# Kernel optimization log

Hardware: AMD Instinct MI355X
Metric: run time of the kernel (lower is better)

## Reference

```python
import jax, jax.numpy as jnp
import numpy as np

F_DIM = 128; K_RBF = 64; NBLOCKS = 3; NUM_SCC = 1; IBEGIN = 4
N_RES_INT = 2; N_RES_AT = 2; N_RES_OUT = 1
NUM_OUTPUTS = 2001; NOUTS = NUM_OUTPUTS + 4  # +4 charge-equilibration channels when num_scc>0
N_ATOMS = 10000; DEG = 32; N_EDGES = N_ATOMS * DEG; NMOL = 64
CUTOFF = 10.0
LOG2 = 0.6931471805599453


def ssp(x):
    # shifted softplus
    return jax.nn.softplus(x) - LOG2


def _residual(x, W1, b1, W2, b2):
    y = ssp(x) @ W1 + b1
    return x + ssp(y) @ W2 + b2


def _forward(R, M, QaAlpha, QaBeta,
             em_W0, em_b0, em_W1, em_b1, em_W2, em_b2,
             iWrbf, iWi, ibi, iWj, ibj, irW1, irb1, irW2, irb2, iWout, ibout, iu,
             arW1, arb1, arW2, arb2, orW1, orb1, orW2, orb2, oW,
             Z, idx_i, idx_j, mol_idx):
    N = R.shape[0]
    dt = R.dtype
    # --- interatomic distances via neighbor gather ---
    Dvec = R[idx_i] - R[idx_j]                                # [E,3]
    Dij = jnp.sqrt(jax.nn.relu(jnp.sum(Dvec * Dvec, -1)))     # [E]
    # --- PhysNet-style exp-Gaussian RBF expansion with smooth cutoff ---
    mu = jnp.linspace(np.exp(-CUTOFF), 1.0, K_RBF).astype(dt)
    gamma = jnp.asarray((K_RBF / (2.0 * (1.0 - np.exp(-CUTOFF)))) ** 2, dt)
    t = Dij / CUTOFF
    cut = jnp.where(Dij < CUTOFF, 1.0 - 6.0 * t**5 + 15.0 * t**4 - 10.0 * t**3, 0.0)
    rbf = cut[:, None] * jnp.exp(-gamma * (jnp.exp(-Dij)[:, None] - mu) ** 2)  # [E,K]

    seg_mol = lambda v: jax.ops.segment_sum(v, mol_idx, num_segments=NMOL)
    Zf = Z.astype(dt)[:, None]
    QaA, QaB = QaAlpha, QaBeta
    QAlpha_mol = seg_mol(QaA)
    QBeta_mol = seg_mol(QaB)
    outputs = None
    nhloss = jnp.asarray(0.0, dt)
    for j in range(NUM_SCC + 1):
        # elemental-modes embedding: f = [Z, M, QaAlpha, QaBeta] -> F
        f = jnp.concatenate([Zf, M[:, None], QaA[:, None], QaB[:, None]], 1)  # [N,4]
        h = ssp(f @ em_W0 + em_b0)
        h = ssp(h @ em_W1 + em_b1)
        x = h @ em_W2 + em_b2                                 # [N,F]
        outputs = jnp.zeros((N, NOUTS), dt)
        nhloss = jnp.asarray(0.0, dt)
        lastout2 = None
        for i in range(NBLOCKS):
            # --- interaction (message passing: gather -> multiply -> segment_sum) ---
            xa = ssp(x)
            g = rbf @ iWrbf[i]                                # [E,F]
            xi = ssp(xa @ iWi[i] + ibi[i])                    # [N,F]
            xj = ssp(xa @ iWj[i] + ibj[i])                    # [N,F]
            m = xi + jax.ops.segment_sum(g * xj[idx_j], idx_i, num_segments=N)
            for r in range(N_RES_INT):
                m = _residual(m, irW1[i, r], irb1[i, r], irW2[i, r], irb2[i, r])
            m = ssp(m)
            x = iu[i] * x + m @ iWout[i] + ibout[i]           # gated update
            for r in range(N_RES_AT):
                x = _residual(x, arW1[i, r], arb1[i, r], arW2[i, r], arb2[i, r])
            # --- output block ---
            xo = x
            for r in range(N_RES_OUT):
                xo = _residual(xo, orW1[i, r], orb1[i, r], orW2[i, r], orb2[i, r])
            out = ssp(xo) @ oW[i]                             # [N,NOUTS]
            outputs = outputs + out
            if j == NUM_SCC:
                out2 = out[IBEGIN:] ** 2                      # row slice, as in source
                if i > 0:
                    nhloss = nhloss + jnp.mean(out2 / (out2 + lastout2 + 1e-7))
                lastout2 = out2
        # --- NSE charge equilibration (per-molecule segment sums) ---
        QaA_n, faA = outputs[:, 0], outputs[:, 1]
        QaB_n, faB = outputs[:, 2], outputs[:, 3]
        QaA = QaA_n + faA * ((QAlpha_mol - seg_mol(QaA_n)) / seg_mol(faA))[mol_idx]
        QaB = QaB_n + faB * ((QBeta_mol - seg_mol(QaB_n)) / seg_mol(faB))[mol_idx]
    outputs = outputs[:, IBEGIN:]
    outputs = jnp.concatenate([outputs[:, :1], jax.nn.relu(outputs[:, 1:])], 1)
    return outputs, Dij, nhloss


def setup_inputs() -> dict:
    key = jax.random.key(0)
    ks = iter(jax.random.split(key, 64))
    nrm = lambda shp, scale: jax.random.normal(next(ks), shp, jnp.float32) * scale
    F, K, B = F_DIM, K_RBF, NBLOCKS
    s = F ** -0.5
    inp = {}
    inp["R"] = jax.random.uniform(next(ks), (N_ATOMS, 3), jnp.float32, 0.0, 12.0)
    inp["M"] = jax.random.uniform(next(ks), (N_ATOMS,), jnp.float32, 1.0, 32.0)
    inp["QaAlpha"] = nrm((N_ATOMS,), 0.1)
    inp["QaBeta"] = nrm((N_ATOMS,), 0.1)
    # elemental-modes MLP 4 -> F -> F -> F
    inp["em_W0"] = nrm((4, F), 0.5); inp["em_b0"] = nrm((F,), 0.01)
    inp["em_W1"] = nrm((F, F), s);   inp["em_b1"] = nrm((F,), 0.01)
    inp["em_W2"] = nrm((F, F), s);   inp["em_b2"] = nrm((F,), 0.01)
    # interaction blocks (stacked over NBLOCKS)
    inp["iWrbf"] = nrm((B, K, F), K ** -0.5)
    inp["iWi"] = nrm((B, F, F), s); inp["ibi"] = nrm((B, F), 0.01)
    inp["iWj"] = nrm((B, F, F), s); inp["ibj"] = nrm((B, F), 0.01)
    inp["irW1"] = nrm((B, N_RES_INT, F, F), s); inp["irb1"] = nrm((B, N_RES_INT, F), 0.01)
    inp["irW2"] = nrm((B, N_RES_INT, F, F), s); inp["irb2"] = nrm((B, N_RES_INT, F), 0.01)
    inp["iWout"] = nrm((B, F, F), s); inp["ibout"] = nrm((B, F), 0.01)
    inp["iu"] = jnp.ones((B, F), jnp.float32)
    inp["arW1"] = nrm((B, N_RES_AT, F, F), s); inp["arb1"] = nrm((B, N_RES_AT, F), 0.01)
    inp["arW2"] = nrm((B, N_RES_AT, F, F), s); inp["arb2"] = nrm((B, N_RES_AT, F), 0.01)
    inp["orW1"] = nrm((B, N_RES_OUT, F, F), s); inp["orb1"] = nrm((B, N_RES_OUT, F), 0.01)
    inp["orW2"] = nrm((B, N_RES_OUT, F, F), s); inp["orb2"] = nrm((B, N_RES_OUT, F), 0.01)
    inp["oW"] = nrm((B, F, NOUTS), s)
    # integer graph structure
    inp["Z"] = jax.random.randint(next(ks), (N_ATOMS,), 1, 36, jnp.int32)
    idx_i = jnp.repeat(jnp.arange(N_ATOMS, dtype=jnp.int32), DEG)
    rnd = jax.random.randint(next(ks), (N_EDGES,), 1, N_ATOMS, jnp.int32)
    inp["idx_i"] = idx_i
    inp["idx_j"] = (idx_i + rnd) % N_ATOMS  # never self -> Dij > 0
    inp["mol_idx"] = ((jnp.arange(N_ATOMS) * NMOL) // N_ATOMS).astype(jnp.int32)
    return inp


def reference(R, M, QaAlpha, QaBeta,
              em_W0, em_b0, em_W1, em_b1, em_W2, em_b2,
              iWrbf, iWi, ibi, iWj, ibj, irW1, irb1, irW2, irb2, iWout, ibout, iu,
              arW1, arb1, arW2, arb2, orW1, orb1, orW2, orb2, oW,
              Z, idx_i, idx_j, mol_idx):
    return _forward(R, M, QaAlpha, QaBeta,
                    em_W0, em_b0, em_W1, em_b1, em_W2, em_b2,
                    iWrbf, iWi, ibi, iWj, ibj, irW1, irb1, irW2, irb2, iWout, ibout, iu,
                    arW1, arb1, arW2, arb2, orW1, orb1, orW2, orb2, oW,
                    Z, idx_i, idx_j, mol_idx)
```

## Files before the change

### kernel.cpp

```cpp
#include <hip/hip_runtime.h>
#include <math.h>

#define NA 10000
#define FD 128
#define KR 64
#define DEGC 32
#define NE (NA*DEGC)
#define NOUTS_C 2005
#define NOUT_FINAL 2001

typedef __attribute__((ext_vector_type(8))) short bh8;
typedef __attribute__((ext_vector_type(4))) float fx4;

__device__ __forceinline__ float sspf(float x){
    float ex = __expf(-fabsf(x));
    return fmaxf(x, 0.0f) + __logf(1.0f + ex) - 0.6931471805599453f;
}
__device__ __forceinline__ unsigned short f2bf(float x){
    unsigned int u = __float_as_uint(x);
    unsigned int r = (u + 0x7fffu + ((u >> 16) & 1u)) >> 16;
    return (unsigned short)r;
}
__device__ __forceinline__ float bf2f(unsigned short u){
    return __uint_as_float(((unsigned int)u) << 16);
}
__device__ __forceinline__ fx4 mfma16(bh8 a, bh8 b, fx4 c){
    return __builtin_amdgcn_mfma_f32_16x16x32_bf16(a, b, c, 0, 0, 0);
}
__device__ __forceinline__ void gll16(const void* g, void* l){
    __builtin_amdgcn_global_load_lds(
        (const __attribute__((address_space(1))) unsigned int*)g,
        (__attribute__((address_space(3))) unsigned int*)l, 16, 0, 0);
}

__global__ void k_dij(const float* __restrict__ R, const int* __restrict__ idx_i,
                      const int* __restrict__ idx_j, float* __restrict__ dij_out){
    int e = blockIdx.x*256 + threadIdx.x;
    if (e >= NE) return;
    int i = idx_i[e], j = idx_j[e];
    float dx = R[i*3+0] - R[j*3+0];
    float dy = R[i*3+1] - R[j*3+1];
    float dz = R[i*3+2] - R[j*3+2];
    dij_out[e] = sqrtf(fmaxf(dx*dx + dy*dy + dz*dz, 0.0f));
}

__global__ void k_init(const float* __restrict__ QaAin, const float* __restrict__ QaBin,
                       const int* __restrict__ mol, float* __restrict__ QaA,
                       float* __restrict__ QaB, float* __restrict__ QAmol,
                       float* __restrict__ QBmol){
    int a = blockIdx.x*256 + threadIdx.x;
    if (a >= NA) return;
    float qa = QaAin[a], qb = QaBin[a];
    QaA[a] = qa; QaB[a] = qb;
    int m = mol[a];
    atomicAdd(&QAmol[m], qa);
    atomicAdd(&QBmol[m], qb);
}

__global__ void k_cvtW(const float* __restrict__ em_W1, const float* __restrict__ em_W2,
                       const float* __restrict__ iWi, const float* __restrict__ iWj,
                       const float* __restrict__ iWout, const float* __restrict__ irW1,
                       const float* __restrict__ irW2, const float* __restrict__ arW1,
                       const float* __restrict__ arW2, const float* __restrict__ orW1,
                       const float* __restrict__ orW2, short* __restrict__ img){
    int gid = blockIdx.x*256 + threadIdx.x;
    if (gid >= 41*2048) return;
    int m = gid >> 11;
    int f = gid & 2047;
    int l15 = f & 15, t = f >> 4;
    int g = t & 3, u = t >> 2;
    int kk = u & 3, cg = u >> 2;
    const float* src; int mm;
    if      (m < 1){ src = em_W1; mm = m; }
    else if (m < 2){ src = em_W2; mm = m-1; }
    else if (m < 5){ src = iWi;   mm = m-2; }
    else if (m < 8){ src = iWj;   mm = m-5; }
    else if (m < 11){ src = iWout; mm = m-8; }
    else if (m < 17){ src = irW1;  mm = m-11; }
    else if (m < 23){ src = irW2;  mm = m-17; }
    else if (m < 29){ src = arW1;  mm = m-23; }
    else if (m < 35){ src = arW2;  mm = m-29; }
    else if (m < 38){ src = orW1;  mm = m-35; }
    else            { src = orW2;  mm = m-38; }
    src += (size_t)mm * 16384;
    int n = cg*16 + l15;
    int k0 = (kk*4 + g)*8;
    bh8 pk;
    #pragma unroll
    for (int j = 0; j < 8; ++j) pk[j] = (short)f2bf(src[(k0+j)*128 + n]);
    *(bh8*)&img[m*16384 + f*8] = pk;
}

__global__ void k_cvtB(const float* __restrict__ em_b1, const float* __restrict__ em_b2,
                       const float* __restrict__ ibi, const float* __restrict__ ibj,
                       const float* __restrict__ ibout, const float* __restrict__ irb1,
                       const float* __restrict__ irb2, const float* __restrict__ arb1,
                       const float* __restrict__ arb2, const float* __restrict__ orb1,
                       const float* __restrict__ orb2, const float* __restrict__ iu,
                       float* __restrict__ bimg){
    int gid = blockIdx.x*256 + threadIdx.x;
    if (gid >= 44*128) return;
    int m = gid >> 7, c = gid & 127;
    float v;
    if      (m < 1)  v = em_b1[c];
    else if (m < 2)  v = em_b2[c];
    else if (m < 5)  v = ibi[(m-2)*128+c];
    else if (m < 8)  v = ibj[(m-5)*128+c];
    else if (m < 11) v = ibout[(m-8)*128+c];
    else if (m < 17) v = irb1[(m-11)*128+c];
    else if (m < 23) v = irb2[(m-17)*128+c];
    else if (m < 29) v = arb1[(m-23)*128+c];
    else if (m < 35) v = arb2[(m-29)*128+c];
    else if (m < 38) v = orb1[(m-35)*128+c];
    else if (m < 41) v = orb2[(m-38)*128+c];
    else             v = iu[(m-41)*128+c];
    bimg[gid] = v;
}

__global__ void k_cvt_wrbf(const float* __restrict__ iWrbf, short* __restrict__ img){
    int gid = blockIdx.x*256 + threadIdx.x;
    if (gid >= 3*1024) return;
    int i = gid >> 10;
    int loc = gid & 1023;
    int n = loc >> 3, s = loc & 7;
    const float* src = iWrbf + (size_t)i*8192;
    int kbase = (s ^ (n&7)) * 8;
    bh8 pk;
    #pragma unroll
    for (int j = 0; j < 8; ++j) pk[j] = (short)f2bf(src[(kbase+j)*128 + n]);
    *(bh8*)&img[i*8192 + n*64 + s*8] = pk;
}

__global__ void k_cvt_oW(const float* __restrict__ oW, short* __restrict__ img){
    int gid = blockIdx.x*256 + threadIdx.x;
    if (gid >= 98304) return;
    int l15 = gid & 15;
    int g = (gid >> 4) & 3;
    int nt = (gid >> 6) & 7;
    int rest = gid >> 9;
    int kk2 = rest % 12, cg = rest / 12;
    int seg = kk2 >> 2;
    int n = cg*128 + nt*16 + l15;
    int kbase = (kk2 & 3)*32 + g*8;
    bh8 pk;
    #pragma unroll
    for (int j = 0; j < 8; ++j){
        float v = (n < NOUTS_C) ? oW[((size_t)seg*128 + kbase + j)*NOUTS_C + n] : 0.0f;
        pk[j] = (short)f2bf(v);
    }
    *(bh8*)&img[(size_t)gid*8] = pk;
}

__device__ __forceinline__ void loadB8(const short* __restrict__ W, int g, int l15, int wv, bh8 b[8]){
    const bh8* Wf = (const bh8*)W;
    const int cgA = wv*2, cgB = wv*2 + 1;
    #pragma unroll
    for (int kk = 0; kk < 4; ++kk){
        b[kk]   = Wf[((cgA*4+kk)*4+g)*16 + l15];
        b[4+kk] = Wf[((cgB*4+kk)*4+g)*16 + l15];
    }
}
__device__ __forceinline__ void gemmB(const short* As, const bh8 b[8], int g, int l15, fx4 acc[2]){
    #pragma unroll
    for (int kk = 0; kk < 4; ++kk){
        int q = kk*4 + g;
        bh8 a = *(const bh8*)&As[l15*128 + ((q ^ (l15&7))*8)];
        acc[0] = mfma16(a, b[kk],   acc[0]);
        acc[1] = mfma16(a, b[4+kk], acc[1]);
    }
}
#define ZACC2 { acc[0]=(fx4){0,0,0,0}; acc[1]=(fx4){0,0,0,0}; }

__device__ __forceinline__ void epiS_ts(short* dst, fx4 acc[2], const float* b,
                                        int g, int c0, int c1){
    float b0 = b[c0], b1 = b[c1];
    #pragma unroll
    for (int r = 0; r < 4; ++r){
        int row = g*4 + r;
        dst[row*128 + (((c0>>3) ^ (row&7))*8) + (c0&7)] = (short)f2bf(sspf(acc[0][r] + b0));
        dst[row*128 + (((c1>>3) ^ (row&7))*8) + (c1&7)] = (short)f2bf(sspf(acc[1][r] + b1));
    }
}
__device__ __forceinline__ void epiS_xadd(float xr[2][4], fx4 acc[2], const float* b,
                                          int c0, int c1){
    float b0 = b[c0], b1 = b[c1];
    #pragma unroll
    for (int r = 0; r < 4; ++r){
        xr[0][r] += acc[0][r] + b0;
        xr[1][r] += acc[1][r] + b1;
    }
}
__device__ __forceinline__ void writeS_xr(short* dst, float xr[2][4], int g, int c0, int c1){
    #pragma unroll
    for (int r = 0; r < 4; ++r){
        int row = g*4 + r;
        dst[row*128 + (((c0>>3) ^ (row&7))*8) + (c0&7)] = (short)f2bf(sspf(xr[0][r]));
        dst[row*128 + (((c1>>3) ^ (row&7))*8) + (c1&7)] = (short)f2bf(sspf(xr[1][r]));
    }
}
__device__ __forceinline__ void storeS_xr(float* dst, float xr[2][4], int r0, int g, int c0, int c1){
    #pragma unroll
    for (int r = 0; r < 4; ++r){
        int row = r0 + g*4 + r;
        dst[(size_t)row*FD + c0] = xr[0][r];
        dst[(size_t)row*FD + c1] = xr[1][r];
    }
}
__device__ __forceinline__ void storeS_ssp(float* dst, fx4 acc[2], const float* b,
                                           int r0, int g, int c0, int c1){
    float b0 = b[c0], b1 = b[c1];
    #pragma unroll
    for (int r = 0; r < 4; ++r){
        int row = r0 + g*4 + r;
        dst[(size_t)row*FD + c0] = sspf(acc[0][r] + b0);
        dst[(size_t)row*FD + c1] = sspf(acc[1][r] + b1);
    }
}
__device__ __forceinline__ void stage_A16(short* As, const float* src, int r0, int tid){
    int row = tid >> 4, cb = tid & 15;
    const float* p = src + (size_t)(r0+row)*FD + cb*8;
    float4 u = *(const float4*)p, v = *(const float4*)(p+4);
    float vv[8] = {u.x,u.y,u.z,u.w,v.x,v.y,v.z,v.w};
    bh8 pk;
    #pragma unroll
    for (int t = 0; t < 8; ++t) pk[t] = (short)f2bf(sspf(vv[t]));
    *(bh8*)&As[row*128 + ((cb ^ (row&7))*8)] = pk;
}

__global__ __launch_bounds__(256) void k_pre(
    const short* __restrict__ wimg, const float* __restrict__ bimg,
    const int* __restrict__ Z, const float* __restrict__ M,
    const float* __restrict__ QaA, const float* __restrict__ QaB,
    const float* __restrict__ em_W0, const float* __restrict__ em_b0,
    float* __restrict__ x, float* __restrict__ xi, float* __restrict__ xj)
{
    __shared__ __align__(16) short As[2048];
    __shared__ __align__(16) short Ts[2048];
    __shared__ float fs[16][4];
    const int tid = threadIdx.x, wv = tid>>6, ln = tid&63, g = ln>>4, l15 = ln&15;
    const int r0 = blockIdx.x*16;
    const int c0 = wv*32 + l15, c1 = c0 + 16;
    bh8 bU[8], bV[8];
    if (tid < 64){
        int rr = tid>>2, k = tid&3;
        int a = r0 + rr;
        fs[rr][k] = (k==0) ? (float)Z[a] : (k==1) ? M[a] : (k==2) ? QaA[a] : QaB[a];
    }
    __syncthreads();
    {
        int row = tid>>4, cb = tid&15;
        bh8 pk;
        #pragma unroll
        for (int t = 0; t < 8; ++t){
            int c = cb*8 + t;
            float v = sspf(em_b0[c] + fs[row][0]*em_W0[c] + fs[row][1]*em_W0[128+c]
                           + fs[row][2]*em_W0[256+c] + fs[row][3]*em_W0[384+c]);
            pk[t] = (short)f2bf(v);
        }
        *(bh8*)&As[row*128 + ((cb ^ (row&7))*8)] = pk;
    }
    loadB8(wimg + 0*16384, g, l15, wv, bU);
    __syncthreads();
    fx4 acc[2];
    float xr[2][4];
    ZACC2; gemmB(As, bU, g, l15, acc);
    loadB8(wimg + 1*16384, g, l15, wv, bV);
    epiS_ts(Ts, acc, bimg + 0*128, g, c0, c1);
    __syncthreads();
    ZACC2; gemmB(Ts, bV, g, l15, acc);
    loadB8(wimg + 2*16384, g, l15, wv, bU);
    {
        const float* b = bimg + 1*128;
        float b0 = b[c0], b1 = b[c1];
        #pragma unroll
        for (int r = 0; r < 4; ++r){
            xr[0][r] = acc[0][r] + b0;
            xr[1][r] = acc[1][r] + b1;
        }
    }
    storeS_xr(x, xr, r0, g, c0, c1);
    writeS_xr(As, xr, g, c0, c1);
    __syncthreads();
    ZACC2; gemmB(As, bU, g, l15, acc);
    loadB8(wimg + 5*16384, g, l15, wv, bV);
    storeS_ssp(xi, acc, bimg + 2*128, r0, g, c0, c1);
    ZACC2; gemmB(As, bV, g, l15, acc);
    storeS_ssp(xj, acc, bimg + 5*128, r0, g, c0, c1);
}

__global__ __launch_bounds__(256) void k_post(
    const short* __restrict__ wimg, const float* __restrict__ bimg,
    const float* __restrict__ mb, float* __restrict__ x,
    short* __restrict__ Aimg, float* __restrict__ xi, float* __restrict__ xj,
    int i, int dodual)
{
    __shared__ __align__(16) short As[2048];
    __shared__ __align__(16) short Ts[2048];
    const int tid = threadIdx.x, wv = tid>>6, ln = tid&63, g = ln>>4, l15 = ln&15;
    const int r0 = blockIdx.x*16;
    const int c0 = wv*32 + l15, c1 = c0 + 16;
    bh8 bU[8], bV[8];
    float xr[2][4];
    #pragma unroll
    for (int r = 0; r < 4; ++r){
        size_t row = (size_t)(r0 + g*4 + r);
        xr[0][r] = mb[row*FD + c0];
        xr[1][r] = mb[row*FD + c1];
    }
    stage_A16(As, mb, r0, tid);
    loadB8(wimg + (size_t)(11+2*i)*16384, g, l15, wv, bU);
    __syncthreads();
    fx4 acc[2];
    ZACC2; gemmB(As, bU, g, l15, acc);
    loadB8(wimg + (size_t)(17+2*i)*16384, g, l15, wv, bV);
    epiS_ts(Ts, acc, bimg + (11+2*i)*128, g, c0, c1);
    __syncthreads();
    ZACC2; gemmB(Ts, bV, g, l15, acc);
    loadB8(wimg + (size_t)(12+2*i)*16384, g, l15, wv, bU);
    epiS_xadd(xr, acc, bimg + (17+2*i)*128, c0, c1);
    writeS_xr(As, xr, g, c0, c1);
    __syncthreads();
    ZACC2; gemmB(As, bU, g, l15, acc);
    loadB8(wimg + (size_t)(18+2*i)*16384, g, l15, wv, bV);
    epiS_ts(Ts, acc, bimg + (12+2*i)*128, g, c0, c1);
    __syncthreads();
    ZACC2; gemmB(Ts, bV, g, l15, acc);
    loadB8(wimg + (size_t)(8+i)*16384, g, l15, wv, bU);
    epiS_xadd(xr, acc, bimg + (18+2*i)*128, c0, c1);
    writeS_xr(As, xr, g, c0, c1);
    __syncthreads();
    ZACC2; gemmB(As, bU, g, l15, acc);
    loadB8(wimg + (size_t)(23+2*i)*16384, g, l15, wv, bV);
    {
        const float* bb = bimg + (8+i)*128;
        const float* uu = bimg + (41+i)*128;
        float b0 = bb[c0], b1 = bb[c1], u0 = uu[c0], u1 = uu[c1];
        #pragma unroll
        for (int r = 0; r < 4; ++r){
            size_t row = (size_t)(r0 + g*4 + r);
            xr[0][r] = u0*x[row*FD + c0] + acc[0][r] + b0;
            xr[1][r] = u1*x[row*FD + c1] + acc[1][r] + b1;
        }
    }
    writeS_xr(Ts, xr, g, c0, c1);
    __syncthreads();
    ZACC2; gemmB(Ts, bV, g, l15, acc);
    loadB8(wimg + (size_t)(29+2*i)*16384, g, l15, wv, bU);
    epiS_ts(As, acc, bimg + (23+2*i)*128, g, c0, c1);
    __syncthreads();
    ZACC2; gemmB(As, bU, g, l15, acc);
    loadB8(wimg + (size_t)(24+2*i)*16384, g, l15, wv, bV);
    epiS_xadd(xr, acc, bimg + (29+2*i)*128, c0, c1);
    writeS_xr(Ts, xr, g, c0, c1);
    __syncthreads();
    ZACC2; gemmB(Ts, bV, g, l15, acc);
    loadB8(wimg + (size_t)(30+2*i)*16384, g, l15, wv, bU);
    epiS_ts(As, acc, bimg + (24+2*i)*128, g, c0, c1);
    __syncthreads();
    ZACC2; gemmB(As, bU, g, l15, acc);
    loadB8(wimg + (size_t)(dodual ? (3+i) : (35+i))*16384, g, l15, wv, bV);
    epiS_xadd(xr, acc, bimg + (30+2*i)*128, c0, c1);
    storeS_xr(x, xr, r0, g, c0, c1);
    writeS_xr(Ts, xr, g, c0, c1);
    __syncthreads();
    if (dodual){
        ZACC2; gemmB(Ts, bV, g, l15, acc);
        loadB8(wimg + (size_t)(6+i)*16384, g, l15, wv, bU);
        storeS_ssp(xi, acc, bimg + (3+i)*128, r0, g, c0, c1);
        ZACC2; gemmB(Ts, bU, g, l15, acc);
        loadB8(wimg + (size_t)(35+i)*16384, g, l15, wv, bV);
        storeS_ssp(xj, acc, bimg + (6+i)*128, r0, g, c0, c1);
        ZACC2; gemmB(Ts, bV, g, l15, acc);
        loadB8(wimg + (size_t)(38+i)*16384, g, l15, wv, bU);
        epiS_ts(As, acc, bimg + (35+i)*128, g, c0, c1);
    } else {
        ZACC2; gemmB(Ts, bV, g, l15, acc);
        loadB8(wimg + (size_t)(38+i)*16384, g, l15, wv, bU);
        epiS_ts(As, acc, bimg + (35+i)*128, g, c0, c1);
    }
    __syncthreads();
    ZACC2; gemmB(As, bU, g, l15, acc);
    {
        const float* bb = bimg + (38+i)*128;
        float b0 = bb[c0], b1 = bb[c1];
        #pragma unroll
        for (int r = 0; r < 4; ++r){
            int row = r0 + g*4 + r;
            float v0 = xr[0][r] + acc[0][r] + b0;
            float v1 = xr[1][r] + acc[1][r] + b1;
            int k0 = i*128 + c0, k1 = i*128 + c1;
            Aimg[(size_t)row*384 + (((k0>>3) ^ (row&7))*8) + (k0&7)] = (short)f2bf(sspf(v0));
            Aimg[(size_t)row*384 + (((k1>>3) ^ (row&7))*8) + (k1&7)] = (short)f2bf(sspf(v1));
        }
    }
}

__global__ __launch_bounds__(256) void k_agg_mfma(
    const float* __restrict__ dij, const short* __restrict__ wri,
    const int* __restrict__ idxj, const float* __restrict__ xi,
    const float* __restrict__ xj, float* __restrict__ mout,
    float gamma, float mu0, float dmu)
{
    __shared__ short Rb[256*64];
    __shared__ short Wr[128*64];
    __shared__ int Jd[256];
    const int tid = threadIdx.x;
    const int wv = tid >> 6, ln = tid & 63;
    const int e0 = blockIdx.x * 256;
    {
        const char* g2 = (const char*)wri;
        char* l2 = (char*)Wr;
        #pragma unroll
        for (int i = 0; i < 4; ++i){
            int off = wv*4096 + i*1024;
            gll16(g2 + off + ln*16, l2 + off);
        }
        Jd[tid] = idxj[e0 + tid];
    }
    {
        float d = dij[e0 + tid];
        float t = d * 0.1f;
        float cut = 0.0f;
        if (d < 10.0f){
            float t2 = t*t, t3 = t2*t, t4 = t2*t2, t5 = t4*t;
            cut = 1.0f - 6.0f*t5 + 15.0f*t4 - 10.0f*t3;
// ... 108 lines not shown
        p2 += __shfl_down(p2, off);
        p3 += __shfl_down(p3, off);
    }
    if (lane == 0){
        out4[a*4+0] = p0; out4[a*4+1] = p1;
        out4[a*4+2] = p2; out4[a*4+3] = p3;
    }
}

__global__ void k_molsum(const float* __restrict__ out4, const int* __restrict__ mol,
                         float* __restrict__ sums){
    int a = blockIdx.x*256 + threadIdx.x;
    if (a >= NA) return;
    int m = mol[a];
    atomicAdd(&sums[m],     out4[a*4+0]);
    atomicAdd(&sums[64+m],  out4[a*4+1]);
    atomicAdd(&sums[128+m], out4[a*4+2]);
    atomicAdd(&sums[192+m], out4[a*4+3]);
}

__global__ void k_qaupd(const float* __restrict__ out4, const int* __restrict__ mol,
                        const float* __restrict__ sums, const float* __restrict__ QAmol,
                        const float* __restrict__ QBmol, float* __restrict__ QaA,
                        float* __restrict__ QaB){
    int a = blockIdx.x*256 + threadIdx.x;
    if (a >= NA) return;
    int m = mol[a];
    float qa_n = out4[a*4+0], fa = out4[a*4+1];
    float qb_n = out4[a*4+2], fb = out4[a*4+3];
    QaA[a] = qa_n + fa * ((QAmol[m] - sums[m])     / sums[64+m]);
    QaB[a] = qb_n + fb * ((QBmol[m] - sums[128+m]) / sums[192+m]);
}

__global__ __launch_bounds__(256) void k_final3(
    const short* __restrict__ Aimg, const short* __restrict__ oWfrag,
    float* __restrict__ outp, float* __restrict__ nh_acc)
{
    __shared__ __align__(16) short As[64*384];
    const int tid = threadIdx.x, wv = tid>>6, ln = tid&63, g = ln>>4, l15 = ln&15;
    const int a0 = blockIdx.x * 64;
    const int cg = blockIdx.y;
    {
        const char* gA = (const char*)(Aimg + (size_t)a0*384);
        char* lA = (char*)As;
        #pragma unroll
        for (int i = 0; i < 12; ++i){
            int off = wv*12288 + i*1024;
            gll16(gA + off + ln*16, lA + off);
        }
    }
    __syncthreads();
    const bh8* Bf = (const bh8*)oWfrag + (size_t)cg*12*8*64;
    const int arow = wv*16 + l15;
    fx4 osum[8], p2[8];
    #pragma unroll
    for (int nt = 0; nt < 8; ++nt){ osum[nt] = (fx4){0,0,0,0}; p2[nt] = (fx4){0,0,0,0}; }
    float nh = 0.f;
    for (int seg = 0; seg < 3; ++seg){
        fx4 acc[8];
        #pragma unroll
        for (int nt = 0; nt < 8; ++nt) acc[nt] = (fx4){0,0,0,0};
        #pragma unroll
        for (int kkl = 0; kkl < 4; ++kkl){
            int kk2 = seg*4 + kkl;
            bh8 b[8];
            #pragma unroll
            for (int nt = 0; nt < 8; ++nt)
                b[nt] = Bf[((size_t)kk2*8 + nt)*64 + g*16 + l15];
            int s = kk2*4 + g;
            bh8 a = *(const bh8*)&As[arow*384 + ((s ^ (arow&7))*8)];
            #pragma unroll
            for (int nt = 0; nt < 8; ++nt)
                acc[nt] = mfma16(a, b[nt], acc[nt]);
        }
        #pragma unroll
        for (int nt = 0; nt < 8; ++nt)
        #pragma unroll
        for (int r = 0; r < 4; ++r){
            float o = acc[nt][r];
            osum[nt][r] += o;
            if (seg > 0){
                int A = a0 + wv*16 + g*4 + r;
                int col = cg*128 + nt*16 + l15;
                if (A >= 4 && A < NA && col < NOUTS_C){
                    float o2 = o*o;
                    float den = o2 + p2[nt][r] + 1e-7f;
                    float rr;
                    asm("v_rcp_f32 %0, %1" : "=v"(rr) : "v"(den));
                    nh += o2 * rr;
                }
            }
            p2[nt][r] = o*o;
        }
    }
    #pragma unroll
    for (int nt = 0; nt < 8; ++nt){
        int col = cg*128 + nt*16 + l15;
        #pragma unroll
        for (int r = 0; r < 4; ++r){
            int A = a0 + wv*16 + g*4 + r;
            if (A < NA && col >= 4 && col < NOUTS_C){
                float v = osum[nt][r];
                if (col > 4) v = fmaxf(v, 0.f);
                outp[(size_t)A*NOUT_FINAL + (col - 4)] = v;
            }
        }
    }
    #pragma unroll
    for (int off = 32; off > 0; off >>= 1) nh += __shfl_down(nh, off);
    if (ln == 0) atomicAdd(nh_acc, nh);
}

__global__ void k_finalize(const float* __restrict__ nh_acc, float* __restrict__ nh_out){
    *nh_out = *nh_acc * (1.0f / (float)((NA - 4) * NOUTS_C));
}

extern "C" void kernel_launch(void* const* d_in, const int* in_sizes, int n_in,
                              void* d_out, int out_size, void* d_ws, size_t ws_size,
                              hipStream_t stream)
{
    const float* R       = (const float*)d_in[0];
    const float* M       = (const float*)d_in[1];
    const float* QaAlpha = (const float*)d_in[2];
    const float* QaBeta  = (const float*)d_in[3];
    const float* em_W0   = (const float*)d_in[4];
    const float* em_b0   = (const float*)d_in[5];
    const float* em_W1   = (const float*)d_in[6];
    const float* em_b1   = (const float*)d_in[7];
    const float* em_W2   = (const float*)d_in[8];
    const float* em_b2   = (const float*)d_in[9];
    const float* iWrbf   = (const float*)d_in[10];
    const float* iWi     = (const float*)d_in[11];
    const float* ibi     = (const float*)d_in[12];
    const float* iWj     = (const float*)d_in[13];
    const float* ibj     = (const float*)d_in[14];
    const float* irW1    = (const float*)d_in[15];
    const float* irb1    = (const float*)d_in[16];
    const float* irW2    = (const float*)d_in[17];
    const float* irb2    = (const float*)d_in[18];
    const float* iWout   = (const float*)d_in[19];
    const float* ibout   = (const float*)d_in[20];
    const float* iu      = (const float*)d_in[21];
    const float* arW1    = (const float*)d_in[22];
    const float* arb1    = (const float*)d_in[23];
    const float* arW2    = (const float*)d_in[24];
    const float* arb2    = (const float*)d_in[25];
    const float* orW1    = (const float*)d_in[26];
    const float* orb1    = (const float*)d_in[27];
    const float* orW2    = (const float*)d_in[28];
    const float* orb2    = (const float*)d_in[29];
    const float* oW      = (const float*)d_in[30];
    const int*   Z       = (const int*)d_in[31];
    const int*   idx_i   = (const int*)d_in[32];
    const int*   idx_j   = (const int*)d_in[33];
    const int*   mol     = (const int*)d_in[34];

    float* out    = (float*)d_out;
    float* dij    = out + (size_t)NA*NOUT_FINAL;
    float* nh_out = dij + NE;

    float* fbase = (float*)d_ws;
    size_t fo = 0;
    float* x    = fbase + fo; fo += (size_t)NA*FD;
    float* xi   = fbase + fo; fo += (size_t)NA*FD;
    float* xj   = fbase + fo; fo += (size_t)NA*FD;
    float* mb   = fbase + fo; fo += (size_t)NA*FD;
    float* out4 = fbase + fo; fo += (size_t)NA*4;
    float* sums = fbase + fo; fo += 256;
    float* QAmol= fbase + fo; fo += 64;
    float* QBmol= fbase + fo; fo += 64;
    float* nhac = fbase + fo; fo += 1;
    float* QaA  = fbase + fo; fo += NA;
    float* QaB  = fbase + fo; fo += NA;
    float* bimg = fbase + fo; fo += 44*128;
    size_t sboff = ((fo*4 + 63) / 64) * 64;
    short* sbase = (short*)((char*)d_ws + sboff);
    size_t so = 0;
    short* wimg   = sbase + so; so += (size_t)41*16384;
    short* wrbf   = sbase + so; so += (size_t)3*8192;
    short* oWfrag = sbase + so; so += (size_t)98304*8;
    short* Aimg   = sbase + so; so += (size_t)10048*384;

    hipMemsetAsync(sums, 0, (size_t)(256 + 64 + 64 + 1)*sizeof(float), stream);
    hipMemsetAsync(Aimg + (size_t)10000*384, 0, (size_t)48*384*sizeof(short), stream);

    k_cvtW<<<(41*2048+255)/256, 256, 0, stream>>>(em_W1, em_W2, iWi, iWj, iWout,
                                                  irW1, irW2, arW1, arW2, orW1, orW2, wimg);
    k_cvtB<<<(44*128+255)/256, 256, 0, stream>>>(em_b1, em_b2, ibi, ibj, ibout,
                                                 irb1, irb2, arb1, arb2, orb1, orb2, iu, bimg);
    k_cvt_wrbf<<<(3*1024+255)/256, 256, 0, stream>>>(iWrbf, wrbf);
    k_cvt_oW<<<(98304+255)/256, 256, 0, stream>>>(oW, oWfrag);

    k_dij<<<(NE+255)/256, 256, 0, stream>>>(R, idx_i, idx_j, dij);
    k_init<<<(NA+255)/256, 256, 0, stream>>>(QaAlpha, QaBeta, mol, QaA, QaB, QAmol, QBmol);

    double expn = exp(-10.0);
    float gamma = (float)pow(64.0/(2.0*(1.0-expn)), 2.0);
    float mu0 = (float)expn;
    float dmu = (float)((1.0-expn)/63.0);

    for (int j = 0; j <= 1; ++j){
        k_pre<<<625, 256, 0, stream>>>(wimg, bimg, Z, M, QaA, QaB, em_W0, em_b0, x, xi, xj);
        for (int i = 0; i < 3; ++i){
            k_agg_mfma<<<1250, 256, 0, stream>>>(dij, wrbf + (size_t)i*8192, idx_j, xi, xj, mb,
                                                 gamma, mu0, dmu);
            k_post<<<625, 256, 0, stream>>>(wimg, bimg, mb, x, Aimg, xi, xj, i, (i<2) ? 1 : 0);
        }
        if (j == 0){
            k_out4all<<<(NA*64)/256, 256, 0, stream>>>(Aimg, oW, out4);
            k_molsum<<<(NA+255)/256, 256, 0, stream>>>(out4, mol, sums);
            k_qaupd<<<(NA+255)/256, 256, 0, stream>>>(out4, mol, sums, QAmol, QBmol, QaA, QaB);
        }
    }
    k_final3<<<dim3(157,16), 256, 0, stream>>>(Aimg, oWfrag, out, nhac);
    k_finalize<<<1, 1, 0, stream>>>(nhac, nh_out);
}
```

Measured before the change: 963.6 us.

## Keep dense MLP chains in registers via transposed MFMA and retile final GEMM

The per-atom dense layers in the pre/post kernels are restructured so each wave owns 16 atoms and all 128 features, computing W^T·x with weights as the A operand. Activations stay in registers as MFMA B fragments across the layer chain, which removes the shared-memory staging and __syncthreads between layers; the weight image layout is rearranged to match. The final output GEMM is retiled to 32-atom blocks that loop over 8 column groups, with waves split over rows and column halves. The trade-off is more register pressure, fewer blocks (157) in the pre/post kernels, and full weight reloads per wave.

```diff
diff --git a/kernel.cpp b/kernel.cpp
--- a/kernel.cpp
+++ b/kernel.cpp
@@ -2,6 +2,7 @@
 #include <math.h>
 
 #define NA 10000
+#define NAP 10048
 #define FD 128
 #define KR 64
 #define DEGC 32
@@ -31,6 +32,63 @@
     __builtin_amdgcn_global_load_lds(
         (const __attribute__((address_space(1))) unsigned int*)g,
         (__attribute__((address_space(3))) unsigned int*)l, 16, 0, 0);
+}
+__device__ __forceinline__ fx4 ssp4(fx4 v){
+    fx4 r;
+    #pragma unroll
+    for (int t = 0; t < 4; ++t) r[t] = sspf(v[t]);
+    return r;
+}
+__device__ __forceinline__ bh8 pk2(fx4 a, fx4 b){
+    bh8 p;
+    #pragma unroll
+    for (int t = 0; t < 4; ++t){ p[t] = (short)f2bf(a[t]); p[4+t] = (short)f2bf(b[t]); }
+    return p;
+}
+
+__device__ __forceinline__ void rgemm(const short* __restrict__ W, const bh8 bfr[4],
+                                      int g, int l15, fx4 acc[8]){
+    const bh8* Wf = (const bh8*)W;
+    #pragma unroll
+    for (int nt = 0; nt < 8; ++nt){
+        acc[nt] = (fx4){0,0,0,0};
+        #pragma unroll
+        for (int kk = 0; kk < 4; ++kk){
+            bh8 a = Wf[((nt*4+kk)*4+g)*16 + l15];
+            acc[nt] = mfma16(a, bfr[kk], acc[nt]);
+        }
+    }
+}
+__device__ __forceinline__ void mkfr(const fx4 y[8], bh8 bfr[4]){
+    #pragma unroll
+    for (int kk = 0; kk < 4; ++kk) bfr[kk] = pk2(y[2*kk], y[2*kk+1]);
+}
+__device__ __forceinline__ void e_ssp(const float* __restrict__ bb, int g, const fx4 acc[8],
+                                      fx4 y[8], bh8 bfr[4]){
+    #pragma unroll
+    for (int nt = 0; nt < 8; ++nt){
+        fx4 b = *(const fx4*)(bb + nt*16 + g*4);
+        y[nt] = ssp4(acc[nt] + b);
+    }
+    mkfr(y, bfr);
+}
+__device__ __forceinline__ void e_xadd(const float* __restrict__ bb, int g, const fx4 acc[8],
+                                       fx4 xr[8], fx4 y[8], bh8 bfr[4]){
+    #pragma unroll
+    for (int nt = 0; nt < 8; ++nt){
+        fx4 b = *(const fx4*)(bb + nt*16 + g*4);
+        xr[nt] += acc[nt] + b;
+        y[nt] = ssp4(xr[nt]);
+    }
+    mkfr(y, bfr);
+}
+__device__ __forceinline__ void st_ssp(float* __restrict__ dst, size_t arow,
+                                       const float* __restrict__ bb, int g, const fx4 acc[8]){
+    #pragma unroll
+    for (int nt = 0; nt < 8; ++nt){
+        fx4 b = *(const fx4*)(bb + nt*16 + g*4);
+        *(fx4*)(dst + arow + nt*16 + g*4) = ssp4(acc[nt] + b);
+    }
 }
 
 __global__ void k_dij(const float* __restrict__ R, const int* __restrict__ idx_i,
@@ -67,9 +125,7 @@
     if (gid >= 41*2048) return;
     int m = gid >> 11;
     int f = gid & 2047;
-    int l15 = f & 15, t = f >> 4;
-    int g = t & 3, u = t >> 2;
-    int kk = u & 3, cg = u >> 2;
+    int l15 = f & 15, g = (f>>4)&3, kk = (f>>6)&3, nt = f>>8;
     const float* src; int mm;
     if      (m < 1){ src = em_W1; mm = m; }
     else if (m < 2){ src = em_W2; mm = m-1; }
@@ -83,11 +139,13 @@
     else if (m < 38){ src = orW1;  mm = m-35; }
     else            { src = orW2;  mm = m-38; }
     src += (size_t)mm * 16384;
-    int n = cg*16 + l15;
-    int k0 = (kk*4 + g)*8;
+    int n = nt*16 + l15;
     bh8 pk;
     #pragma unroll
-    for (int j = 0; j < 8; ++j) pk[j] = (short)f2bf(src[(k0+j)*128 + n]);
+    for (int j = 0; j < 8; ++j){
+        int k = (2*kk + (j>>2))*16 + g*4 + (j&3);
+        pk[j] = (short)f2bf(src[k*128 + n]);
+    }
     *(bh8*)&img[m*16384 + f*8] = pk;
 }
 
@@ -151,246 +209,122 @@
     *(bh8*)&img[(size_t)gid*8] = pk;
 }
 
-__device__ __forceinline__ void loadB8(const short* __restrict__ W, int g, int l15, int wv, bh8 b[8]){
-    const bh8* Wf = (const bh8*)W;
-    const int cgA = wv*2, cgB = wv*2 + 1;
-    #pragma unroll
-    for (int kk = 0; kk < 4; ++kk){
-        b[kk]   = Wf[((cgA*4+kk)*4+g)*16 + l15];
-        b[4+kk] = Wf[((cgB*4+kk)*4+g)*16 + l15];
-    }
-}
-__device__ __forceinline__ void gemmB(const short* As, const bh8 b[8], int g, int l15, fx4 acc[2]){
-    #pragma unroll
-    for (int kk = 0; kk < 4; ++kk){
-        int q = kk*4 + g;
-        bh8 a = *(const bh8*)&As[l15*128 + ((q ^ (l15&7))*8)];
-        acc[0] = mfma16(a, b[kk],   acc[0]);
-        acc[1] = mfma16(a, b[4+kk], acc[1]);
-    }
-}
-#define ZACC2 { acc[0]=(fx4){0,0,0,0}; acc[1]=(fx4){0,0,0,0}; }
-
-__device__ __forceinline__ void epiS_ts(short* dst, fx4 acc[2], const float* b,
-                                        int g, int c0, int c1){
-    float b0 = b[c0], b1 = b[c1];
-    #pragma unroll
-    for (int r = 0; r < 4; ++r){
-        int row = g*4 + r;
-        dst[row*128 + (((c0>>3) ^ (row&7))*8) + (c0&7)] = (short)f2bf(sspf(acc[0][r] + b0));
-        dst[row*128 + (((c1>>3) ^ (row&7))*8) + (c1&7)] = (short)f2bf(sspf(acc[1][r] + b1));
-    }
-}
-__device__ __forceinline__ void epiS_xadd(float xr[2][4], fx4 acc[2], const float* b,
-                                          int c0, int c1){
-    float b0 = b[c0], b1 = b[c1];
-    #pragma unroll
-    for (int r = 0; r < 4; ++r){
-        xr[0][r] += acc[0][r] + b0;
-        xr[1][r] += acc[1][r] + b1;
-    }
-}
-__device__ __forceinline__ void writeS_xr(short* dst, float xr[2][4], int g, int c0, int c1){
-    #pragma unroll
-    for (int r = 0; r < 4; ++r){
-        int row = g*4 + r;
-        dst[row*128 + (((c0>>3) ^ (row&7))*8) + (c0&7)] = (short)f2bf(sspf(xr[0][r]));
-        dst[row*128 + (((c1>>3) ^ (row&7))*8) + (c1&7)] = (short)f2bf(sspf(xr[1][r]));
-    }
-}
-__device__ __forceinline__ void storeS_xr(float* dst, float xr[2][4], int r0, int g, int c0, int c1){
-    #pragma unroll
-    for (int r = 0; r < 4; ++r){
-        int row = r0 + g*4 + r;
-        dst[(size_t)row*FD + c0] = xr[0][r];
-        dst[(size_t)row*FD + c1] = xr[1][r];
-    }
-}
-__device__ __forceinline__ void storeS_ssp(float* dst, fx4 acc[2], const float* b,
-                                           int r0, int g, int c0, int c1){
-    float b0 = b[c0], b1 = b[c1];
-    #pragma unroll
-    for (int r = 0; r < 4; ++r){
-        int row = r0 + g*4 + r;
-        dst[(size_t)row*FD + c0] = sspf(acc[0][r] + b0);
-        dst[(size_t)row*FD + c1] = sspf(acc[1][r] + b1);
-    }
-}
-__device__ __forceinline__ void stage_A16(short* As, const float* src, int r0, int tid){
-    int row = tid >> 4, cb = tid & 15;
-    const float* p = src + (size_t)(r0+row)*FD + cb*8;
-    float4 u = *(const float4*)p, v = *(const float4*)(p+4);
-    float vv[8] = {u.x,u.y,u.z,u.w,v.x,v.y,v.z,v.w};
-    bh8 pk;
-    #pragma unroll
-    for (int t = 0; t < 8; ++t) pk[t] = (short)f2bf(sspf(vv[t]));
-    *(bh8*)&As[row*128 + ((cb ^ (row&7))*8)] = pk;
-}
-
-__global__ __launch_bounds__(256) void k_pre(
+__global__ __launch_bounds__(256) void k_pre_r(
     const short* __restrict__ wimg, const float* __restrict__ bimg,
     const int* __restrict__ Z, const float* __restrict__ M,
     const float* __restrict__ QaA, const float* __restrict__ QaB,
     const float* __restrict__ em_W0, const float* __restrict__ em_b0,
     float* __restrict__ x, float* __restrict__ xi, float* __restrict__ xj)
 {
-    __shared__ __align__(16) short As[2048];
-    __shared__ __align__(16) short Ts[2048];
-    __shared__ float fs[16][4];
-    const int tid = threadIdx.x, wv = tid>>6, ln = tid&63, g = ln>>4, l15 = ln&15;
-    const int r0 = blockIdx.x*16;
-    const int c0 = wv*32 + l15, c1 = c0 + 16;
-    bh8 bU[8], bV[8];
-    if (tid < 64){
-        int rr = tid>>2, k = tid&3;
-        int a = r0 + rr;
-        fs[rr][k] = (k==0) ? (float)Z[a] : (k==1) ? M[a] : (k==2) ? QaA[a] : QaB[a];
-    }
-    __syncthreads();
+    const int tid = threadIdx.x, ln = tid & 63, g = ln>>4, l15 = ln & 15;
+    const int atom = blockIdx.x*64 + (tid>>6)*16 + l15;
+    const int aa = (atom < NA) ? atom : (NA-1);
+    const size_t arow = (size_t)atom*FD;
+    float f0 = (float)Z[aa], f1 = M[aa], f2 = QaA[aa], f3 = QaB[aa];
+    fx4 xr[8], y[8], acc[8];
+    bh8 bfr[4];
+    #pragma unroll
+    for (int nt = 0; nt < 8; ++nt){
+        int c = nt*16 + g*4;
+        fx4 b0v = *(const fx4*)(em_b0 + c);
+        fx4 w0 = *(const fx4*)(em_W0 + c);
+        fx4 w1 = *(const fx4*)(em_W0 + 128 + c);
+        fx4 w2 = *(const fx4*)(em_W0 + 256 + c);
+        fx4 w3 = *(const fx4*)(em_W0 + 384 + c);
+        y[nt] = ssp4(b0v + f0*w0 + f1*w1 + f2*w2 + f3*w3);
+    }
+    mkfr(y, bfr);
+    rgemm(wimg + 0*16384, bfr, g, l15, acc);
+    e_ssp(bimg + 0*128, g, acc, y, bfr);
+    rgemm(wimg + 1*16384, bfr, g, l15, acc);
     {
-        int row = tid>>4, cb = tid&15;
-        bh8 pk;
-        #pragma unroll
-        for (int t = 0; t < 8; ++t){
-            int c = cb*8 + t;
-            float v = sspf(em_b0[c] + fs[row][0]*em_W0[c] + fs[row][1]*em_W0[128+c]
-                           + fs[row][2]*em_W0[256+c] + fs[row][3]*em_W0[384+c]);
-            pk[t] = (short)f2bf(v);
-        }
-        *(bh8*)&As[row*128 + ((cb ^ (row&7))*8)] = pk;
-    }
-    loadB8(wimg + 0*16384, g, l15, wv, bU);
-    __syncthreads();
-    fx4 acc[2];
-    float xr[2][4];
-    ZACC2; gemmB(As, bU, g, l15, acc);
-    loadB8(wimg + 1*16384, g, l15, wv, bV);
-    epiS_ts(Ts, acc, bimg + 0*128, g, c0, c1);
-    __syncthreads();
-    ZACC2; gemmB(Ts, bV, g, l15, acc);
-    loadB8(wimg + 2*16384, g, l15, wv, bU);
-    {
-        const float* b = bimg + 1*128;
-        float b0 = b[c0], b1 = b[c1];
-        #pragma unroll
-        for (int r = 0; r < 4; ++r){
-            xr[0][r] = acc[0][r] + b0;
-            xr[1][r] = acc[1][r] + b1;
-        }
-    }
-    storeS_xr(x, xr, r0, g, c0, c1);
-    writeS_xr(As, xr, g, c0, c1);
-    __syncthreads();
-    ZACC2; gemmB(As, bU, g, l15, acc);
-    loadB8(wimg + 5*16384, g, l15, wv, bV);
-    storeS_ssp(xi, acc, bimg + 2*128, r0, g, c0, c1);
-    ZACC2; gemmB(As, bV, g, l15, acc);
-    storeS_ssp(xj, acc, bimg + 5*128, r0, g, c0, c1);
-}
-
-__global__ __launch_bounds__(256) void k_post(
+        const float* bb = bimg + 1*128;
+        #pragma unroll
+        for (int nt = 0; nt < 8; ++nt){
+            fx4 b = *(const fx4*)(bb + nt*16 + g*4);
+            xr[nt] = acc[nt] + b;
+            *(fx4*)(x + arow + nt*16 + g*4) = xr[nt];
+            y[nt] = ssp4(xr[nt]);
+        }
+        mkfr(y, bfr);
+    }
+    rgemm(wimg + 2*16384, bfr, g, l15, acc);
+    st_ssp(xi, arow, bimg + 2*128, g, acc);
+    rgemm(wimg + 5*16384, bfr, g, l15, acc);
+    st_ssp(xj, arow, bimg + 5*128, g, acc);
+}
+
+__global__ __launch_bounds__(256) void k_post_r(
     const short* __restrict__ wimg, const float* __restrict__ bimg,
     const float* __restrict__ mb, float* __restrict__ x,
     short* __restrict__ Aimg, float* __restrict__ xi, float* __restrict__ xj,
     int i, int dodual)
 {
-    __shared__ __align__(16) short As[2048];
-    __shared__ __align__(16) short Ts[2048];
-    const int tid = threadIdx.x, wv = tid>>6, ln = tid&63, g = ln>>4, l15 = ln&15;
-    const int r0 = blockIdx.x*16;
-    const int c0 = wv*32 + l15, c1 = c0 + 16;
-    bh8 bU[8], bV[8];
-    float xr[2][4];
-    #pragma unroll
-    for (int r = 0; r < 4; ++r){
-        size_t row = (size_t)(r0 + g*4 + r);
-        xr[0][r] = mb[row*FD + c0];
-        xr[1][r] = mb[row*FD + c1];
-    }
-    stage_A16(As, mb, r0, tid);
-    loadB8(wimg + (size_t)(11+2*i)*16384, g, l15, wv, bU);
-    __syncthreads();
-    fx4 acc[2];
-    ZACC2; gemmB(As, bU, g, l15, acc);
-    loadB8(wimg + (size_t)(17+2*i)*16384, g, l15, wv, bV);
-    epiS_ts(Ts, acc, bimg + (11+2*i)*128, g, c0, c1);
-    __syncthreads();
-    ZACC2; gemmB(Ts, bV, g, l15, acc);
-    loadB8(wimg + (size_t)(12+2*i)*16384, g, l15, wv, bU);
-    epiS_xadd(xr, acc, bimg + (17+2*i)*128, c0, c1);
-    writeS_xr(As, xr, g, c0, c1);
-    __syncthreads();
-    ZACC2; gemmB(As, bU, g, l15, acc);
-    loadB8(wimg + (size_t)(18+2*i)*16384, g, l15, wv, bV);
-    epiS_ts(Ts, acc, bimg + (12+2*i)*128, g, c0, c1);
-    __syncthreads();
-    ZACC2; gemmB(Ts, bV, g, l15, acc);
-    loadB8(wimg + (size_t)(8+i)*16384, g, l15, wv, bU);
-    epiS_xadd(xr, acc, bimg + (18+2*i)*128, c0, c1);
-    writeS_xr(As, xr, g, c0, c1);
-    __syncthreads();
-    ZACC2; gemmB(As, bU, g, l15, acc);
-    loadB8(wimg + (size_t)(23+2*i)*16384, g, l15, wv, bV);
+    const int tid = threadIdx.x, ln = tid & 63, g = ln>>4, l15 = ln & 15;
+    const int atom = blockIdx.x*64 + (tid>>6)*16 + l15;
+    const size_t arow = (size_t)atom*FD;
+    fx4 xr[8], y[8], acc[8];
+    bh8 bfr[4];
+    #pragma unroll
+    for (int nt = 0; nt < 8; ++nt){
+        xr[nt] = *(const fx4*)(mb + arow + nt*16 + g*4);
+        y[nt] = ssp4(xr[nt]);
+    }
+    mkfr(y, bfr);
+    rgemm(wimg + (size_t)(11+2*i)*16384, bfr, g, l15, acc);
+    e_ssp(bimg + (11+2*i)*128, g, acc, y, bfr);
+    rgemm(wimg + (size_t)(17+2*i)*16384, bfr, g, l15, acc);
+    e_xadd(bimg + (17+2*i)*128, g, acc, xr, y, bfr);
+    rgemm(wimg + (size_t)(12+2*i)*16384, bfr, g, l15, acc);
+    e_ssp(bimg + (12+2*i)*128, g, acc, y, bfr);
+    rgemm(wimg + (size_t)(18+2*i)*16384, bfr, g, l15, acc);
+    e_xadd(bimg + (18+2*i)*128, g, acc, xr, y, bfr);
+    rgemm(wimg + (size_t)(8+i)*16384, bfr, g, l15, acc);
     {
         const float* bb = bimg + (8+i)*128;
         const float* uu = bimg + (41+i)*128;
-        float b0 = bb[c0], b1 = bb[c1], u0 = uu[c0], u1 = uu[c1];
-        #pragma unroll
-        for (int r = 0; r < 4; ++r){
-            size_t row = (size_t)(r0 + g*4 + r);
-            xr[0][r] = u0*x[row*FD + c0] + acc[0][r] + b0;
-            xr[1][r] = u1*x[row*FD + c1] + acc[1][r] + b1;
-        }
-    }
-    writeS_xr(Ts, xr, g, c0, c1);
-    __syncthreads();
-    ZACC2; gemmB(Ts, bV, g, l15, acc);
-    loadB8(wimg + (size_t)(29+2*i)*16384, g, l15, wv, bU);
-    epiS_ts(As, acc, bimg + (23+2*i)*128, g, c0, c1);
-    __syncthreads();
-    ZACC2; gemmB(As, bU, g, l15, acc);
-    loadB8(wimg + (size_t)(24+2*i)*16384, g, l15, wv, bV);
-    epiS_xadd(xr, acc, bimg + (29+2*i)*128, c0, c1);
-    writeS_xr(Ts, xr, g, c0, c1);
-    __syncthreads();
-    ZACC2; gemmB(Ts, bV, g, l15, acc);
-    loadB8(wimg + (size_t)(30+2*i)*16384, g, l15, wv, bU);
-    epiS_ts(As, acc, bimg + (24+2*i)*128, g, c0, c1);
-    __syncthreads();
-    ZACC2; gemmB(As, bU, g, l15, acc);
-    loadB8(wimg + (size_t)(dodual ? (3+i) : (35+i))*16384, g, l15, wv, bV);
-    epiS_xadd(xr, acc, bimg + (30+2*i)*128, c0, c1);
-    storeS_xr(x, xr, r0, g, c0, c1);
-    writeS_xr(Ts, xr, g, c0, c1);
-    __syncthreads();
+        #pragma unroll
+        for (int nt = 0; nt < 8; ++nt){
+            fx4 b = *(const fx4*)(bb + nt*16 + g*4);
+            fx4 u = *(const fx4*)(uu + nt*16 + g*4);
+            fx4 xo = *(const fx4*)(x + arow + nt*16 + g*4);
+            xr[nt] = u*xo + acc[nt] + b;
+            y[nt] = ssp4(xr[nt]);
+        }
+        mkfr(y, bfr);
+    }
+    rgemm(wimg + (size_t)(23+2*i)*16384, bfr, g, l15, acc);
+    e_ssp(bimg + (23+2*i)*128, g, acc, y, bfr);
+    rgemm(wimg + (size_t)(29+2*i)*16384, bfr, g, l15, acc);
+    e_xadd(bimg + (29+2*i)*128, g, acc, xr, y, bfr);
+    rgemm(wimg + (size_t)(24+2*i)*16384, bfr, g, l15, acc);
+    e_ssp(bimg + (24+2*i)*128, g, acc, y, bfr);
+    rgemm(wimg + (size_t)(30+2*i)*16384, bfr, g, l15, acc);
+    e_xadd(bimg + (30+2*i)*128, g, acc, xr, y, bfr);
+    #pragma unroll
+    for (int nt = 0; nt < 8; ++nt)
+        *(fx4*)(x + arow + nt*16 + g*4) = xr[nt];
     if (dodual){
-        ZACC2; gemmB(Ts, bV, g, l15, acc);
-        loadB8(wimg + (size_t)(6+i)*16384, g, l15, wv, bU);
-        storeS_ssp(xi, acc, bimg + (3+i)*128, r0, g, c0, c1);
-        ZACC2; gemmB(Ts, bU, g, l15, acc);
-        loadB8(wimg + (size_t)(35+i)*16384, g, l15, wv, bV);
-        storeS_ssp(xj, acc, bimg + (6+i)*128, r0, g, c0, c1);
-        ZACC2; gemmB(Ts, bV, g, l15, acc);
-        loadB8(wimg + (size_t)(38+i)*16384, g, l15, wv, bU);
-        epiS_ts(As, acc, bimg + (35+i)*128, g, c0, c1);
-    } else {
-        ZACC2; gemmB(Ts, bV, g, l15, acc);
-        loadB8(wimg + (size_t)(38+i)*16384, g, l15, wv, bU);
-        epiS_ts(As, acc, bimg + (35+i)*128, g, c0, c1);
-    }
-    __syncthreads();
-    ZACC2; gemmB(As, bU, g, l15, acc);
+        rgemm(wimg + (size_t)(3+i)*16384, bfr, g, l15, acc);
+        st_ssp(xi, arow, bimg + (3+i)*128, g, acc);
+        rgemm(wimg + (size_t)(6+i)*16384, bfr, g, l15, acc);
+        st_ssp(xj, arow, bimg + (6+i)*128, g, acc);
+    }
+    rgemm(wimg + (size_t)(35+i)*16384, bfr, g, l15, acc);
+    e_ssp(bimg + (35+i)*128, g, acc, y, bfr);
+    rgemm(wimg + (size_t)(38+i)*16384, bfr, g, l15, acc);
     {
         const float* bb = bimg + (38+i)*128;
-        float b0 = bb[c0], b1 = bb[c1];
-        #pragma unroll
-        for (int r = 0; r < 4; ++r){
-            int row = r0 + g*4 + r;
-            float v0 = xr[0][r] + acc[0][r] + b0;
-            float v1 = xr[1][r] + acc[1][r] + b1;
-            int k0 = i*128 + c0, k1 = i*128 + c1;
-            Aimg[(size_t)row*384 + (((k0>>3) ^ (row&7))*8) + (k0&7)] = (short)f2bf(sspf(v0));
-            Aimg[(size_t)row*384 + (((k1>>3) ^ (row&7))*8) + (k1&7)] = (short)f2bf(sspf(v1));
+        #pragma unroll
+        for (int nt = 0; nt < 8; ++nt){
+            fx4 b = *(const fx4*)(bb + nt*16 + g*4);
+            fx4 v = ssp4(xr[nt] + acc[nt] + b);
+            unsigned int u0 = (unsigned int)f2bf(v[0]) | ((unsigned int)f2bf(v[1]) << 16);
+            unsigned int u1 = (unsigned int)f2bf(v[2]) | ((unsigned int)f2bf(v[3]) << 16);
+            int s = i*16 + nt*2 + (g>>1);
+            int idx = atom*384 + ((s ^ (atom&7))*8) + (g&1)*4;
+            *(unsigned int*)&Aimg[idx]   = u0;
+            *(unsigned int*)&Aimg[idx+2] = u1;
         }
     }
 }
@@ -565,77 +499,80 @@
     QaB[a] = qb_n + fb * ((QBmol[m] - sums[128+m]) / sums[192+m]);
 }
 
-__global__ __launch_bounds__(256) void k_final3(
+__global__ __launch_bounds__(256) void k_final4(
     const short* __restrict__ Aimg, const short* __restrict__ oWfrag,
     float* __restrict__ outp, float* __restrict__ nh_acc)
 {
-    __shared__ __align__(16) short As[64*384];
+    __shared__ __align__(16) short As[32*384];
     const int tid = threadIdx.x, wv = tid>>6, ln = tid&63, g = ln>>4, l15 = ln&15;
-    const int a0 = blockIdx.x * 64;
-    const int cg = blockIdx.y;
+    const int a0 = blockIdx.x * 32;
+    const int rt = wv & 1, nth = wv >> 1;
     {
         const char* gA = (const char*)(Aimg + (size_t)a0*384);
         char* lA = (char*)As;
         #pragma unroll
-        for (int i = 0; i < 12; ++i){
-            int off = wv*12288 + i*1024;
+        for (int t = 0; t < 6; ++t){
+            int off = t*4096 + wv*1024;
             gll16(gA + off + ln*16, lA + off);
         }
     }
     __syncthreads();
-    const bh8* Bf = (const bh8*)oWfrag + (size_t)cg*12*8*64;
-    const int arow = wv*16 + l15;
-    fx4 osum[8], p2[8];
-    #pragma unroll
-    for (int nt = 0; nt < 8; ++nt){ osum[nt] = (fx4){0,0,0,0}; p2[nt] = (fx4){0,0,0,0}; }
+    const int arow = rt*16 + l15;
     float nh = 0.f;
-    for (int seg = 0; seg < 3; ++seg){
-        fx4 acc[8];
-        #pragma unroll
-        for (int nt = 0; nt < 8; ++nt) acc[nt] = (fx4){0,0,0,0};
-        #pragma unroll
-        for (int kkl = 0; kkl < 4; ++kkl){
-            int kk2 = seg*4 + kkl;
-            bh8 b[8];
-            #pragma unroll
-            for (int nt = 0; nt < 8; ++nt)
-                b[nt] = Bf[((size_t)kk2*8 + nt)*64 + g*16 + l15];
-            int s = kk2*4 + g;
-            bh8 a = *(const bh8*)&As[arow*384 + ((s ^ (arow&7))*8)];
-            #pragma unroll
-            for (int nt = 0; nt < 8; ++nt)
-                acc[nt] = mfma16(a, b[nt], acc[nt]);
-        }
-        #pragma unroll
-        for (int nt = 0; nt < 8; ++nt)
-        #pragma unroll
-        for (int r = 0; r < 4; ++r){
-            float o = acc[nt][r];
-            osum[nt][r] += o;
-            if (seg > 0){
-                int A = a0 + wv*16 + g*4 + r;
-                int col = cg*128 + nt*16 + l15;
-                if (A >= 4 && A < NA && col < NOUTS_C){
-                    float o2 = o*o;
-                    float den = o2 + p2[nt][r] + 1e-7f;
-                    float rr;
-                    asm("v_rcp_f32 %0, %1" : "=v"(rr) : "v"(den));
-                    nh += o2 * rr;
+    for (int cgl = 0; cgl < 8; ++cgl){
+        int cg = blockIdx.y*8 + cgl;
+        const bh8* Bf = (const bh8*)oWfrag + (size_t)cg*6144;
+        fx4 osum[4], p2[4];
+        #pragma unroll
+        for (int ntl = 0; ntl < 4; ++ntl){ osum[ntl] = (fx4){0,0,0,0}; p2[ntl] = (fx4){0,0,0,0}; }
+        #pragma unroll
+        for (int seg = 0; seg < 3; ++seg){
+            fx4 acc[4];
+            #pragma unroll
+            for (int ntl = 0; ntl < 4; ++ntl) acc[ntl] = (fx4){0,0,0,0};
+            #pragma unroll
+            for (int kkl = 0; kkl < 4; ++kkl){
+                int kk2 = seg*4 + kkl;
+                int s = kk2*4 + g;
+                bh8 a = *(const bh8*)&As[arow*384 + ((s ^ (arow&7))*8)];
+                #pragma unroll
+                for (int ntl = 0; ntl < 4; ++ntl){
+                    int nt = nth*4 + ntl;
+                    bh8 b = Bf[((kk2*8 + nt)*4 + g)*16 + l15];
+                    acc[ntl] = mfma16(a, b, acc[ntl]);
                 }
             }
-            p2[nt][r] = o*o;
-        }
-    }
-    #pragma unroll
-    for (int nt = 0; nt < 8; ++nt){
-        int col = cg*128 + nt*16 + l15;
-        #pragma unroll
-        for (int r = 0; r < 4; ++r){
-            int A = a0 + wv*16 + g*4 + r;
-            if (A < NA && col >= 4 && col < NOUTS_C){
-                float v = osum[nt][r];
-                if (col > 4) v = fmaxf(v, 0.f);
-                outp[(size_t)A*NOUT_FINAL + (col - 4)] = v;
+            #pragma unroll
+            for (int ntl = 0; ntl < 4; ++ntl)
+            #pragma unroll
+            for (int r = 0; r < 4; ++r){
+                float o = acc[ntl][r];
+                osum[ntl][r] += o;
+                if (seg > 0){
+                    int A = a0 + rt*16 + g*4 + r;
+                    int col = cg*128 + (nth*4+ntl)*16 + l15;
+                    if (A >= 4 && A < NA && col < NOUTS_C){
+                        float o2 = o*o;
+                        float den = o2 + p2[ntl][r] + 1e-7f;
+                        float rr;
+                        asm("v_rcp_f32 %0, %1" : "=v"(rr) : "v"(den));
+                        nh += o2 * rr;
+                    }
+                }
+                p2[ntl][r] = o*o;
+            }
+        }
+        #pragma unroll
+        for (int ntl = 0; ntl < 4; ++ntl){
+            int col = cg*128 + (nth*4+ntl)*16 + l15;
+            #pragma unroll
+            for (int r = 0; r < 4; ++r){
+                int A = a0 + rt*16 + g*4 + r;
+                if (A < NA && col >= 4 && col < NOUTS_C){
+                    float v = osum[ntl][r];
+                    if (col > 4) v = fmaxf(v, 0.f);
+                    outp[(size_t)A*NOUT_FINAL + (col - 4)] = v;
+                }
             }
         }
     }
@@ -694,10 +631,10 @@
 
     float* fbase = (float*)d_ws;
     size_t fo = 0;
-    float* x    = fbase + fo; fo += (size_t)NA*FD;
-    float* xi   = fbase + fo; fo += (size_t)NA*FD;
-    float* xj   = fbase + fo; fo += (size_t)NA*FD;
-    float* mb   = fbase + fo; fo += (size_t)NA*FD;
+    float* x    = fbase + fo; fo += (size_t)NAP*FD;
+    float* xi   = fbase + fo; fo += (size_t)NAP*FD;
+    float* xj   = fbase + fo; fo += (size_t)NAP*FD;
+    float* mb   = fbase + fo; fo += (size_t)NAP*FD;
     float* out4 = fbase + fo; fo += (size_t)NA*4;
     float* sums = fbase + fo; fo += 256;
     float* QAmol= fbase + fo; fo += 64;
@@ -712,10 +649,9 @@
     short* wimg   = sbase + so; so += (size_t)41*16384;
     short* wrbf   = sbase + so; so += (size_t)3*8192;
     short* oWfrag = sbase + so; so += (size_t)98304*8;
-    short* Aimg   = sbase + so; so += (size_t)10048*384;
+    short* Aimg   = sbase + so; so += (size_t)NAP*384;
 
     hipMemsetAsync(sums, 0, (size_t)(256 + 64 + 64 + 1)*sizeof(float), stream);
-    hipMemsetAsync(Aimg + (size_t)10000*384, 0, (size_t)48*384*sizeof(short), stream);
 
     k_cvtW<<<(41*2048+255)/256, 256, 0, stream>>>(em_W1, em_W2, iWi, iWj, iWout,
                                                   irW1, irW2, arW1, arW2, orW1, orW2, wimg);
@@ -733,11 +669,11 @@
     float dmu = (float)((1.0-expn)/63.0);
 
     for (int j = 0; j <= 1; ++j){
-        k_pre<<<625, 256, 0, stream>>>(wimg, bimg, Z, M, QaA, QaB, em_W0, em_b0, x, xi, xj);
+        k_pre_r<<<157, 256, 0, stream>>>(wimg, bimg, Z, M, QaA, QaB, em_W0, em_b0, x, xi, xj);
         for (int i = 0; i < 3; ++i){
             k_agg_mfma<<<1250, 256, 0, stream>>>(dij, wrbf + (size_t)i*8192, idx_j, xi, xj, mb,
                                                  gamma, mu0, dmu);
-            k_post<<<625, 256, 0, stream>>>(wimg, bimg, mb, x, Aimg, xi, xj, i, (i<2) ? 1 : 0);
+            k_post_r<<<157, 256, 0, stream>>>(wimg, bimg, mb, x, Aimg, xi, xj, i, (i<2) ? 1 : 0);
         }
         if (j == 0){
             k_out4all<<<(NA*64)/256, 256, 0, stream>>>(Aimg, oW, out4);
@@ -745,6 +681,6 @@
             k_qaupd<<<(NA+255)/256, 256, 0, stream>>>(out4, mol, sums, QAmol, QBmol, QaA, QaB);
         }
     }
-    k_final3<<<dim3(157,16), 256, 0, stream>>>(Aimg, oWfrag, out, nhac);
+    k_final4<<<dim3(314,2), 256, 0, stream>>>(Aimg, oWfrag, out, nhac);
     k_finalize<<<1, 1, 0, stream>>>(nhac, nh_out);
 }
```

Measured after the change: 1.774 ms. 1.84x slower.
